# Optimization experiments

Measured on AMD Instinct MI355X. Metric: run time of the kernel, lower is better.

Reference implementation:

```python
import jax, jax.numpy as jnp
import numpy as np
from jax import lax

# LiteMSA config: in_ch=256, out_ch=256, dim=8, heads=32, total_dim=256, scales=(3,)
DIM = 8
QKV_CH = 768          # 3 * total_dim
PW_GROUPS = 96        # 3 * heads


def setup_inputs() -> dict:
    key = jax.random.key(0)
    ks = jax.random.split(key, 5)
    x = jax.random.normal(ks[0], (16, 256, 64, 64), jnp.float32)
    w_qkv = jax.random.normal(ks[1], (768, 256), jnp.float32) * 0.02      # 1x1 conv
    w_dw = jax.random.normal(ks[2], (768, 1, 3, 3), jnp.float32) * 0.02   # depthwise 3x3
    w_pw = jax.random.normal(ks[3], (768, 8, 1, 1), jnp.float32) * 0.02   # grouped 1x1, 96 groups
    w_proj = jax.random.normal(ks[4], (256, 512), jnp.float32) * 0.02     # 1x1 conv
    bn_gamma = jnp.ones((256,), jnp.float32)
    bn_beta = jnp.zeros((256,), jnp.float32)
    bn_mean = jnp.zeros((256,), jnp.float32)
    bn_var = jnp.ones((256,), jnp.float32)
    return {"x": x, "w_qkv": w_qkv, "w_dw": w_dw, "w_pw": w_pw, "w_proj": w_proj,
            "bn_gamma": bn_gamma, "bn_beta": bn_beta, "bn_mean": bn_mean, "bn_var": bn_var}


def reference(x, w_qkv, w_dw, w_pw, w_proj, bn_gamma, bn_beta, bn_mean, bn_var):
    B, _, H, W = x.shape
    dn = ("NCHW", "OIHW", "NCHW")
    # qkv 1x1 conv
    qkv = jnp.einsum("bchw,oc->bohw", x, w_qkv)  # [B,768,H,W]
    # multi-scale aggregation: depthwise 3x3 -> grouped 1x1
    agg = lax.conv_general_dilated(qkv, w_dw, (1, 1), "SAME",
                                   dimension_numbers=dn, feature_group_count=QKV_CH)
    agg = lax.conv_general_dilated(agg, w_pw, (1, 1), "SAME",
                                   dimension_numbers=dn, feature_group_count=PW_GROUPS)
    ms = jnp.concatenate([qkv, agg], axis=1)  # [B,1536,H,W]
    # [B, heads_total=64, N=H*W, 3*dim]
    ms = ms.reshape(B, -1, 3 * DIM, H * W).transpose(0, 1, 3, 2)
    q = jax.nn.relu(ms[..., :DIM])
    k = jax.nn.relu(ms[..., DIM:2 * DIM])
    v = ms[..., 2 * DIM:]
    # pad v with ones for normalizer channel
    v = jnp.concatenate([v, jnp.ones(v.shape[:-1] + (1,), v.dtype)], axis=-1)  # [B,h,N,dim+1]
    kv = jnp.einsum("bhnd,bhne->bhde", k, v)   # [B,h,dim,dim+1]
    out = jnp.einsum("bhnd,bhde->bhne", q, kv)  # [B,h,N,dim+1]
    out = out[..., :DIM] / (out[..., DIM:] + 1e-15)
    out = out.transpose(0, 1, 3, 2).reshape(B, -1, H, W)  # [B,512,H,W]
    # proj 1x1 conv + BatchNorm (inference, running stats)
    y = jnp.einsum("bchw,oc->bohw", out, w_proj)
    inv = bn_gamma / jnp.sqrt(bn_var + 1e-5)
    y = y * inv[None, :, None, None] + (bn_beta - bn_mean * inv)[None, :, None, None]
    return y
```

## Files before the change

### kernel.cpp

```cpp
#include <hip/hip_runtime.h>
#include <hip/hip_bf16.h>


#define NB 16
#define CQKV 768
#define P4096 4096
#define QFIX_CAP (1u << 21)

typedef __bf16 bf16x8 __attribute__((ext_vector_type(8)));
typedef float f32x4 __attribute__((ext_vector_type(4)));

#define MFMA_BF16 __builtin_amdgcn_mfma_f32_16x16x32_bf16

__device__ __forceinline__ ushort f2bf(float f) {
    union { float f; unsigned int u; } x; x.f = f;
    unsigned int u = x.u;
    unsigned int r = (u + 0x7FFFu + ((u >> 16) & 1u)) >> 16;
    return (ushort)r;
}
__device__ __forceinline__ float bf2f(ushort u) {
    union { unsigned int u; float f; } x; x.u = ((unsigned int)u) << 16;
    return x.f;
}
__device__ __forceinline__ unsigned int pk2bf(float x, float y) {
    __hip_bfloat162 h = __float22bfloat162_rn(make_float2(x, y));
    union { __hip_bfloat162 b; unsigned int u; } c; c.b = h; return c.u;
}
__device__ __forceinline__ void stage_hi8(const float* v, ushort* dh) {
    union { unsigned int u[4]; uint4 q; } H;
    #pragma unroll
    for (int i = 0; i < 4; i++) H.u[i] = pk2bf(v[2 * i], v[2 * i + 1]);
    *(uint4*)dh = H.q;
}

__device__ __forceinline__ void gload16(void* lds, const void* g) {
    __builtin_amdgcn_global_load_lds(
        (const __attribute__((address_space(1))) void*)g,
        (__attribute__((address_space(3))) void*)lds, 16, 0, 0);
}

__global__ __launch_bounds__(128) void conv_w(
    const float* __restrict__ W, ushort* __restrict__ Ah, ushort* __restrict__ Al)
{
    const int rv = blockIdx.x;
    const int t  = threadIdx.x;
    int phys;
    if (rv < 256) phys = (rv >> 3) * 24 + (rv & 7);
    else { int r2 = rv - 256; phys = (r2 >> 4) * 24 + 8 + (r2 & 15); }
    int c = t * 2;
    float w0 = W[(size_t)phys * 256 + c];
    float w1 = W[(size_t)phys * 256 + c + 1];
    unsigned int h = pk2bf(w0, w1);
    float f0 = __uint_as_float(h << 16);
    float f1 = __uint_as_float(h & 0xffff0000u);
    unsigned int l = pk2bf(w0 - f0, w1 - f1);
    int sl = ((c >> 3) & 3) ^ ((rv >> 1) & 3);
    int idx = (c & ~31) + sl * 8 + (c & 7);
    *(unsigned int*)&Ah[(size_t)rv * 256 + idx] = h;
    *(unsigned int*)&Al[(size_t)rv * 256 + idx] = l;
}

__global__ __launch_bounds__(256) void conv_x(
    const float* __restrict__ X, ushort* __restrict__ XTh, ushort* __restrict__ XTl)
{
    const int pt = blockIdx.x;
    const int ct = blockIdx.y;
    const int b  = blockIdx.z;
    const int t  = threadIdx.x;
    const int p0 = pt * 64, c0 = ct * 64;

    __shared__ float tile[64][65];

    {
        int cr = t >> 2, pc = (t & 3) * 16;
        const float* xr = X + ((size_t)b * 256 + c0 + cr) * P4096 + p0 + pc;
        float4 v0 = *(const float4*)xr;
        float4 v1 = *(const float4*)(xr + 4);
        float4 v2 = *(const float4*)(xr + 8);
        float4 v3 = *(const float4*)(xr + 12);
        float* d = &tile[cr][pc];
        d[0]=v0.x; d[1]=v0.y; d[2]=v0.z; d[3]=v0.w;
        d[4]=v1.x; d[5]=v1.y; d[6]=v1.z; d[7]=v1.w;
        d[8]=v2.x; d[9]=v2.y; d[10]=v2.z; d[11]=v2.w;
        d[12]=v3.x; d[13]=v3.y; d[14]=v3.z; d[15]=v3.w;
    }
    __syncthreads();

    #pragma unroll
    for (int pass = 0; pass < 2; pass++) {
        int tp = t >> 2;
        int cc = (t & 3) + pass * 4;
        int p  = p0 + tp;
        float v[8];
        #pragma unroll
        for (int j = 0; j < 8; j++) v[j] = tile[cc * 8 + j][tp];
        union { unsigned int u[4]; uint4 q; } H, L;
        #pragma unroll
        for (int i = 0; i < 4; i++) {
            unsigned int h = pk2bf(v[2 * i], v[2 * i + 1]);
            H.u[i] = h;
            float f0 = __uint_as_float(h << 16);
            float f1 = __uint_as_float(h & 0xffff0000u);
            L.u[i] = pk2bf(v[2 * i] - f0, v[2 * i + 1] - f1);
        }
        int c = c0 + cc * 8;
        int sl = ((c >> 3) & 3) ^ ((p >> 1) & 3);
        size_t idx = ((size_t)b * P4096 + p) * 256 + (c & ~31) + sl * 8;
        *(uint4*)&XTh[idx] = H.q;
        *(uint4*)&XTl[idx] = L.q;
    }
}

__global__ void zero_cnt(unsigned int* qmeta) { if (threadIdx.x == 0) qmeta[0] = 0; }

__global__ __launch_bounds__(256, 2) void gemm_fused(
    const ushort* __restrict__ Ah, const ushort* __restrict__ Al,
    const ushort* __restrict__ Bh, const ushort* __restrict__ Bl,
    ushort* __restrict__ Cbf, float* __restrict__ qplane,
    unsigned int* __restrict__ qmeta)
{
    const int hw = blockIdx.x;
    const int lg = (hw & 7) * 384 + (hw >> 3);
    const int mt = lg % 6;
    const int rem = lg / 6;
    const int n0 = (rem & 31) * 128;
    const int b  = rem >> 5;
    const int t  = threadIdx.x;
    const int wave = t >> 6, lane = t & 63, quad = lane >> 4, l15 = lane & 15;
    const int wr = wave >> 1, wc = wave & 1;
    const int M0 = mt * 128;

    __shared__ __align__(16) ushort AsH[2][4096];
    __shared__ __align__(16) ushort AsL[2][4096];
    __shared__ __align__(16) ushort BsH[2][4096];
    __shared__ __align__(16) ushort BsL[2][4096];

    int aoff[4], boff[4];
    #pragma unroll
    for (int i = 0; i < 4; i++) {
        int ra = wr * 64 + i * 16 + l15;
        aoff[i] = ra * 64 + ((quad ^ ((ra >> 1) & 3)) << 4);
        int rb = wc * 64 + i * 16 + l15;
        boff[i] = rb * 64 + ((quad ^ ((rb >> 1) & 3)) << 4);
    }

    const int srow = t >> 2;
    const int schunk = (t & 3) * 8;
    const size_t abase = (size_t)(M0 + srow) * 256 + schunk;
    const size_t bbase = ((size_t)b * P4096 + n0 + srow) * 256 + schunk;
    const int ldsoff = wave * 1024;

    f32x4 acc[4][4];
    #pragma unroll
    for (int mi = 0; mi < 4; mi++)
        #pragma unroll
        for (int nj = 0; nj < 4; nj++)
            #pragma unroll
            for (int r = 0; r < 4; r++) acc[mi][nj][r] = 0.0f;

    if (mt < 2) {
        auto stageQ = [&](int d, int kw) {
            #pragma unroll
            for (int i = 0; i < 2; i++) {
                int lo = ldsoff + i * 4096;
                size_t so = (size_t)(i * 64) * 256 + (size_t)kw * 32;
                gload16((char*)AsH[d] + lo, Ah + abase + so);
                gload16((char*)AsL[d] + lo, Al + abase + so);
                gload16((char*)BsH[d] + lo, Bh + bbase + so);
                gload16((char*)BsL[d] + lo, Bl + bbase + so);
            }
        };
        stageQ(0, 0);
        for (int kw = 0; kw < 8; kw++) {
            int cur = kw & 1;
            if (kw < 7) {
                stageQ(cur ^ 1, kw + 1);
                asm volatile("s_waitcnt vmcnt(8)" ::: "memory");
            } else {
                asm volatile("s_waitcnt vmcnt(0)" ::: "memory");
            }
            __builtin_amdgcn_s_barrier();
            bf16x8 ah[4], al[4];
            #pragma unroll
            for (int mi = 0; mi < 4; mi++) {
                ah[mi] = *(const bf16x8*)((const char*)AsH[cur] + aoff[mi]);
                al[mi] = *(const bf16x8*)((const char*)AsL[cur] + aoff[mi]);
            }
            #pragma unroll
            for (int nj = 0; nj < 4; nj++) {
                bf16x8 bh = *(const bf16x8*)((const char*)BsH[cur] + boff[nj]);
                bf16x8 bl = *(const bf16x8*)((const char*)BsL[cur] + boff[nj]);
                #pragma unroll
                for (int mi = 0; mi < 4; mi++) {
                    acc[mi][nj] = MFMA_BF16(ah[mi], bh, acc[mi][nj], 0, 0, 0);
                    acc[mi][nj] = MFMA_BF16(al[mi], bh, acc[mi][nj], 0, 0, 0);
                    acc[mi][nj] = MFMA_BF16(ah[mi], bl, acc[mi][nj], 0, 0, 0);
                }
            }
            __builtin_amdgcn_s_barrier();
        }
        unsigned int* qlist = qmeta + 16;
        #pragma unroll
        for (int mi = 0; mi < 4; mi++)
            #pragma unroll
            for (int nj = 0; nj < 4; nj++)
                #pragma unroll
                for (int r = 0; r < 4; r++) {
                    int rv = M0 + wr * 64 + mi * 16 + quad * 4 + r;
                    int rp = (rv >> 3) * 24 + (rv & 7);
                    int col = n0 + wc * 64 + nj * 16 + l15;
                    float v = acc[mi][nj][r];
                    Cbf[((size_t)b * CQKV + rp) * P4096 + col] = f2bf(v);
                    qplane[((size_t)b * 256 + rv) * P4096 + col] = v;
                    if (fabsf(v) < 1e-4f) {
                        unsigned int idx = atomicAdd(qmeta, 1u);
                        if (idx < QFIX_CAP)
                            qlist[idx] = (unsigned int)(((b * 256 + rv) << 12) | col);
                    }
                }
    } else {
        auto stageKV = [&](int d, int kw) {
            #pragma unroll
            for (int i = 0; i < 2; i++) {
                int lo = ldsoff + i * 4096;
                size_t so = (size_t)(i * 64) * 256 + (size_t)kw * 32;
                gload16((char*)AsH[d] + lo, Ah + abase + so);
                gload16((char*)BsH[d] + lo, Bh + bbase + so);
            }
        };
        stageKV(0, 0);
        for (int kw = 0; kw < 8; kw++) {
            int cur = kw & 1;
            if (kw < 7) {
                stageKV(cur ^ 1, kw + 1);
                asm volatile("s_waitcnt vmcnt(4)" ::: "memory");
            } else {
                asm volatile("s_waitcnt vmcnt(0)" ::: "memory");
            }
            __builtin_amdgcn_s_barrier();
            bf16x8 ah[4];
            #pragma unroll
            for (int mi = 0; mi < 4; mi++)
                ah[mi] = *(const bf16x8*)((const char*)AsH[cur] + aoff[mi]);
            #pragma unroll
            for (int nj = 0; nj < 4; nj++) {
                bf16x8 bh = *(const bf16x8*)((const char*)BsH[cur] + boff[nj]);
                #pragma unroll
                for (int mi = 0; mi < 4; mi++)
                    acc[mi][nj] = MFMA_BF16(ah[mi], bh, acc[mi][nj], 0, 0, 0);
            }
            __builtin_amdgcn_s_barrier();
        }
        #pragma unroll
        for (int mi = 0; mi < 4; mi++)
            #pragma unroll
            for (int nj = 0; nj < 4; nj++)
                #pragma unroll
                for (int r = 0; r < 4; r++) {
                    int rv2 = (M0 - 256) + wr * 64 + mi * 16 + quad * 4 + r;
                    int rp = (rv2 >> 4) * 24 + 8 + (rv2 & 15);
                    int col = n0 + wc * 64 + nj * 16 + l15;
                    Cbf[((size_t)b * CQKV + rp) * P4096 + col] = f2bf(acc[mi][nj][r]);
                }
    }
}

__global__ __launch_bounds__(256) void qfix2_kernel(
    float* __restrict__ qplane, const float* __restrict__ w_qkv,
    const float* __restrict__ x, const unsigned int* __restrict__ qmeta)
{
    unsigned int n = qmeta[0];
    if (n > QFIX_CAP) n = QFIX_CAP;
    const unsigned int* list = qmeta + 16;
    const int wave = threadIdx.x >> 6, lane = threadIdx.x & 63;
    for (unsigned int e = blockIdx.x * 4 + wave; e < n; e += gridDim.x * 4) {
        unsigned int i = list[e];
        int p   = (int)(i & 4095);
        int qch = (int)((i >> 12) & 255);
        int b   = (int)(i >> 20);
        int row = (qch >> 3) * 24 + (qch & 7);
        const float* wr = w_qkv + (size_t)row * 256;
        const float* xr = x + (size_t)b * 256 * P4096 + p;
        double s = 0.0;
        #pragma unroll
        for (int j = 0; j < 4; j++) {
            int c = lane * 4 + j;
            s += (double)wr[c] * (double)xr[(size_t)c * P4096];
        }
        #pragma unroll
        for (int off = 32; off > 0; off >>= 1) s += __shfl_xor(s, off, 64);
        if (lane == 0)
            qplane[((size_t)(b * 256 + qch)) * P4096 + p] = (float)s;
    }
}

__global__ __launch_bounds__(512, 8) void dwpw_kernel(
    const ushort* __restrict__ qkv, const float* __restrict__ wdw,
    const float* __restrict__ wpw, ushort* __restrict__ agg)
{
    const int rt = blockIdx.x;
    const int g  = blockIdx.y;
    const int b  = blockIdx.z;
    const int t  = threadIdx.x;
    const int r0 = rt * 16;
    const int cg = g * 8;

    __shared__ __align__(16) ushort tile[8][18][80];

    const ushort* src = qkv + ((size_t)(b * CQKV + cg)) * P4096;

    if (t < 288) {
        int ch = t / 36;
        int rr = (t % 36) >> 1;
        int side = t & 1;
        *(uint4*)&tile[ch][rr][side * 72] = make_uint4(0, 0, 0, 0);
    }
    #pragma unroll
    for (int i = 0; i < 3; i++) {
        int id = t + i * 512;
        if (id < 1152) {
            int ch  = id / 144;
            int rem = id - ch * 144;
            int rr  = rem >> 3;
            int oct = (rem & 7) * 8;
            int grow = r0 - 1 + rr;
            uint4 v = make_uint4(0, 0, 0, 0);
            if (grow >= 0 && grow < 64)
                v = *(const uint4*)(src + (size_t)ch * P4096 + (size_t)grow * 64 + oct);
            *(uint4*)&tile[ch][rr][8 + oct] = v;
        }
    }
    __syncthreads();

    const int kc  = t & 31;
    const int row = t >> 5;
    const float* wdwg = wdw + (size_t)cg * 9;
    const float* wpwg = wpw + (size_t)cg * 8;

    float acc0[8], acc1[8];
    #pragma unroll
    for (int oi = 0; oi < 8; oi++) { acc0[oi] = 0.0f; acc1[oi] = 0.0f; }

    #pragma unroll
    for (int c = 0; c < 8; c++) {
        float dv0 = 0.0f, dv1 = 0.0f;
        #pragma unroll
        for (int dy = 0; dy < 3; dy++) {
            const ushort* rp = &tile[c][row + dy][2 * kc + 4];
            unsigned int u1 = *(const unsigned int*)(rp + 2);
            unsigned int u2 = *(const unsigned int*)(rp + 4);
            unsigned int u3 = *(const unsigned int*)(rp + 6);
            float xm1 = __uint_as_float(u1 & 0xffff0000u);
            float x0  = __uint_as_float(u2 << 16);
            float x1  = __uint_as_float(u2 & 0xffff0000u);
            float x2  = __uint_as_float(u3 << 16);
            float w0 = wdwg[c * 9 + dy * 3 + 0];
            float w1 = wdwg[c * 9 + dy * 3 + 1];
            float w2 = wdwg[c * 9 + dy * 3 + 2];
            dv0 = fmaf(w0, xm1, dv0); dv0 = fmaf(w1, x0, dv0); dv0 = fmaf(w2, x1, dv0);
            dv1 = fmaf(w0, x0,  dv1); dv1 = fmaf(w1, x1, dv1); dv1 = fmaf(w2, x2, dv1);
        }
        #pragma unroll
        for (int oi = 0; oi < 8; oi++) {
            float w = wpwg[oi * 8 + c];
            acc0[oi] = fmaf(w, dv0, acc0[oi]);
            acc1[oi] = fmaf(w, dv1, acc1[oi]);
        }
    }

    size_t obase = ((size_t)(b * CQKV + cg)) * P4096 + (size_t)(r0 + row) * 64 + 2 * kc;
    #pragma unroll
    for (int oi = 0; oi < 8; oi++) {
        unsigned int u = (unsigned int)f2bf(acc0[oi]) |
                         ((unsigned int)f2bf(acc1[oi]) << 16);
        *(unsigned int*)&agg[obase + (size_t)oi * P4096] = u;
    }
}

__global__ __launch_bounds__(256) void kv_kernel(
    const ushort* __restrict__ qkv, const ushort* __restrict__ agg,
    float* __restrict__ kv)
{
    const int h = blockIdx.x, b = blockIdx.y, t = threadIdx.x;
    const ushort* src = (h < 32)
        ? qkv + ((size_t)(b * CQKV + h * 24)) * P4096
        : agg + ((size_t)(b * CQKV + (h - 32) * 24)) * P4096;

    float acc[72];
    #pragma unroll
    for (int i = 0; i < 72; i++) acc[i] = 0.0f;

    for (int pi = 0; pi < 16; pi++) {
        int p = t + pi * 256;
        float kvv[8], vv[8];
        #pragma unroll
        for (int d = 0; d < 8; d++) {
            float xk = bf2f(src[(size_t)(8 + d) * P4096 + p]);
            kvv[d] = xk > 0.0f ? xk : 0.0f;
        }
        #pragma unroll
        for (int e = 0; e < 8; e++) vv[e] = bf2f(src[(size_t)(16 + e) * P4096 + p]);
        #pragma unroll
        for (int d = 0; d < 8; d++) {
            #pragma unroll
            for (int e = 0; e < 8; e++) acc[d * 9 + e] += kvv[d] * vv[e];
            acc[d * 9 + 8] += kvv[d];
        }
    }

    #pragma unroll
    for (int i = 0; i < 72; i++) {
        float v = acc[i];
        #pragma unroll
        for (int off = 32; off > 0; off >>= 1) v += __shfl_xor(v, off, 64);
        acc[i] = v;
    }
    __shared__ float part[4][72];
    int wave = t >> 6, lane = t & 63;
    if (lane == 0) {
        #pragma unroll
        for (int i = 0; i < 72; i++) part[wave][i] = acc[i];
    }
    __syncthreads();
    if (t < 72)
        kv[((size_t)b * 64 + h) * 72 + t] = part[0][t] + part[1][t] + part[2][t] + part[3][t];
}

__global__ __launch_bounds__(256) void attn_out_kernel(
    const float* __restrict__ qplane, ushort* __restrict__ agg,
    const float* __restrict__ kv)
{
    const int pt = blockIdx.x, h = blockIdx.y, b = blockIdx.z, t = threadIdx.x;
    __shared__ float kvs[72];
    if (t < 72) kvs[t] = kv[((size_t)b * 64 + h) * 72 + t];
    __syncthreads();

    const bool lohead = (h < 32);
    const float* srcf = lohead
        ? qplane + ((size_t)(b * 256 + h * 8)) * P4096 : nullptr;
    const ushort* srcb = lohead ? nullptr
        : agg + ((size_t)(b * CQKV + (h - 32) * 24)) * P4096;

    int p = pt * 256 + t;
    float num[8]; float den = 0.0f;
    #pragma unroll
    for (int e = 0; e < 8; e++) num[e] = 0.0f;
    #pragma unroll
    for (int d = 0; d < 8; d++) {
        float q = lohead ? srcf[(size_t)d * P4096 + p]
                         : bf2f(srcb[(size_t)d * P4096 + p]);
        q = q > 0.0f ? q : 0.0f;
        #pragma unroll
        for (int e = 0; e < 8; e++) num[e] += q * kvs[d * 9 + e];
        den += q * kvs[d * 9 + 8];
    }
    float rd = 1.0f / (den + 1e-15f);
    ushort* dst = agg + ((size_t)(b * CQKV + (h / 2) * 24 + 8 + (h % 2) * 8)) * P4096 + p;
    #pragma unroll
    for (int e = 0; e < 8; e++)
        dst[(size_t)e * P4096] = f2bf(num[e] * rd);
}

__global__ __launch_bounds__(256) void gemm_proj(
    const float* __restrict__ A,
    const ushort* __restrict__ Bagg,
    float* __restrict__ Y,
    const float* __restrict__ bn_g, const float* __restrict__ bn_b,
    const float* __restrict__ bn_m, const float* __restrict__ bn_v)
{
    const int n0 = blockIdx.x * 64;
    const int m0 = blockIdx.y * 64;
    const int b  = blockIdx.z;
    const int t  = threadIdx.x;
    const int wave = t >> 6, lane = t & 63, quad = lane >> 4, l15 = lane & 15;

    __shared__ __align__(16) ushort As[64][40];
    __shared__ __align__(16) ushort Bs[64][40];

    f32x4 acc[4];
    #pragma unroll
    for (int nt = 0; nt < 4; nt++)
        #pragma unroll
        for (int r = 0; r < 4; r++) acc[nt][r] = 0.0f;

    const int am = t >> 2, ak = (t & 3) * 8;
    const int bn = t & 63, kg = (t >> 6) * 8;

    for (int k0 = 0; k0 < 512; k0 += 32) {
        float av[8];
        *(float4*)&av[0] = *(const float4*)(A + (size_t)(m0 + am) * 512 + k0 + ak);
        *(float4*)&av[4] = *(const float4*)(A + (size_t)(m0 + am) * 512 + k0 + ak + 4);
        ushort bu[8];
        #pragma unroll
        for (int i = 0; i < 8; i++) {
            int kk = k0 + kg + i;
            int amch = (kk >> 4) * 24 + 8 + (kk & 15);
            bu[i] = Bagg[((size_t)b * CQKV + amch) * P4096 + n0 + bn];
        }

        __syncthreads();
        stage_hi8(av, &As[am][ak]);
        {
            union { ushort us[8]; uint4 q; } Bp;
            #pragma unroll
            for (int i = 0; i < 8; i++) Bp.us[i] = bu[i];
            *(uint4*)&Bs[bn][kg] = Bp.q;
        }
        __syncthreads();

        bf16x8 af = *(const bf16x8*)&As[wave * 16 + l15][quad * 8];
        #pragma unroll
        for (int nt = 0; nt < 4; nt++) {
            bf16x8 bf = *(const bf16x8*)&Bs[nt * 16 + l15][quad * 8];
            acc[nt] = MFMA_BF16(af, bf, acc[nt], 0, 0, 0);
        }
    }

    #pragma unroll
    for (int nt = 0; nt < 4; nt++) {
        #pragma unroll
        for (int r = 0; r < 4; r++) {
            int row = m0 + wave * 16 + quad * 4 + r;
            int col = n0 + nt * 16 + l15;
            float inv = bn_g[row] / sqrtf(bn_v[row] + 1e-5f);
            float v = acc[nt][r] * inv + (bn_b[row] - bn_m[row] * inv);
            Y[((size_t)b * 256 + row) * P4096 + col] = v;
        }
    }
}

extern "C" void kernel_launch(void* const* d_in, const int* in_sizes, int n_in,
                              void* d_out, int out_size, void* d_ws, size_t ws_size,
                              hipStream_t stream) {
    const float* x      = (const float*)d_in[0];
    const float* w_qkv  = (const float*)d_in[1];
    const float* w_dw   = (const float*)d_in[2];
    const float* w_pw   = (const float*)d_in[3];
    const float* w_proj = (const float*)d_in[4];
    const float* bn_g   = (const float*)d_in[5];
    const float* bn_b   = (const float*)d_in[6];
    const float* bn_m   = (const float*)d_in[7];
    const float* bn_v   = (const float*)d_in[8];
    float* y = (float*)d_out;

    char* ws = (char*)d_ws;
    ushort* qkv_bf = (ushort*)(ws);
    float*  qplane = (float*) (ws + 100663296);
    ushort* agg_bf = (ushort*)(ws + 167772160);
    ushort* XTh = (ushort*)(ws + 167772160);
    ushort* XTl = (ushort*)(ws + 167772160 + 33554432);
    ushort* Awh = (ushort*)(ws + 167772160 + 67108864);
    ushort* Awl = (ushort*)(ws + 167772160 + 67108864 + 393216);
    float*  kvbuf  = (float*)d_out;
    unsigned int* qmeta = (unsigned int*)((char*)d_out + 524288);

    conv_w<<<dim3(768), 128, 0, stream>>>(w_qkv, Awh, Awl);
    zero_cnt<<<1, 64, 0, stream>>>(qmeta);
    conv_x<<<dim3(64, 4, NB), 256, 0, stream>>>(x, XTh, XTl);

    gemm_fused<<<dim3(3072), 256, 0, stream>>>(
        Awh, Awl, XTh, XTl, qkv_bf, qplane, qmeta);

    qfix2_kernel<<<dim3(1024), 256, 0, stream>>>(qplane, w_qkv, x, qmeta);

    dwpw_kernel<<<dim3(4, 96, NB), 512, 0, stream>>>(qkv_bf, w_dw, w_pw, agg_bf);

    kv_kernel<<<dim3(64, NB), 256, 0, stream>>>(qkv_bf, agg_bf, kvbuf);

    attn_out_kernel<<<dim3(16, 64, NB), 256, 0, stream>>>(qplane, agg_bf, kvbuf);

    gemm_proj<<<dim3(64, 4, NB), 256, 0, stream>>>(
        w_proj, agg_bf, y, bn_g, bn_b, bn_m, bn_v);
}
```

Baseline: 411.3 us.

## Retile projection GEMM to 128x128 with double-buffered LDS and pre-converted weights

```diff
diff --git a/kernel.cpp b/kernel.cpp
--- a/kernel.cpp
+++ b/kernel.cpp
@@ -25,12 +25,6 @@
 __device__ __forceinline__ unsigned int pk2bf(float x, float y) {
     __hip_bfloat162 h = __float22bfloat162_rn(make_float2(x, y));
     union { __hip_bfloat162 b; unsigned int u; } c; c.b = h; return c.u;
-}
-__device__ __forceinline__ void stage_hi8(const float* v, ushort* dh) {
-    union { unsigned int u[4]; uint4 q; } H;
-    #pragma unroll
-    for (int i = 0; i < 4; i++) H.u[i] = pk2bf(v[2 * i], v[2 * i + 1]);
-    *(uint4*)dh = H.q;
 }
 
 __device__ __forceinline__ void gload16(void* lds, const void* g) {
@@ -58,6 +52,20 @@
     int idx = (c & ~31) + sl * 8 + (c & 7);
     *(unsigned int*)&Ah[(size_t)rv * 256 + idx] = h;
     *(unsigned int*)&Al[(size_t)rv * 256 + idx] = l;
+}
+
+__global__ __launch_bounds__(256) void conv_wp(
+    const float* __restrict__ W, ushort* __restrict__ Awp)
+{
+    const int m = blockIdx.x;
+    const int t = threadIdx.x;
+    int c = t * 2;
+    float w0 = W[(size_t)m * 512 + c];
+    float w1 = W[(size_t)m * 512 + c + 1];
+    unsigned int h = pk2bf(w0, w1);
+    int sl = ((c >> 3) & 3) ^ ((m >> 1) & 3);
+    int idx = (c & ~31) + sl * 8 + (c & 7);
+    *(unsigned int*)&Awp[(size_t)m * 512 + idx] = h;
 }
 
 __global__ __launch_bounds__(256) void conv_x(
@@ -461,72 +469,118 @@
         dst[(size_t)e * P4096] = f2bf(num[e] * rd);
 }
 
-__global__ __launch_bounds__(256) void gemm_proj(
-    const float* __restrict__ A,
+__global__ __launch_bounds__(256, 2) void gemm_proj(
+    const ushort* __restrict__ Awp,
     const ushort* __restrict__ Bagg,
     float* __restrict__ Y,
     const float* __restrict__ bn_g, const float* __restrict__ bn_b,
     const float* __restrict__ bn_m, const float* __restrict__ bn_v)
 {
-    const int n0 = blockIdx.x * 64;
-    const int m0 = blockIdx.y * 64;
-    const int b  = blockIdx.z;
+    const int hw = blockIdx.x;
+    const int lg = (hw & 7) * 128 + (hw >> 3);
+    const int mt = lg & 1;
+    const int rem = lg >> 1;
+    const int n0 = (rem & 31) * 128;
+    const int b  = rem >> 5;
     const int t  = threadIdx.x;
     const int wave = t >> 6, lane = t & 63, quad = lane >> 4, l15 = lane & 15;
-
-    __shared__ __align__(16) ushort As[64][40];
-    __shared__ __align__(16) ushort Bs[64][40];
-
-    f32x4 acc[4];
-    #pragma unroll
-    for (int nt = 0; nt < 4; nt++)
-        #pragma unroll
-        for (int r = 0; r < 4; r++) acc[nt][r] = 0.0f;
-
-    const int am = t >> 2, ak = (t & 3) * 8;
-    const int bn = t & 63, kg = (t >> 6) * 8;
-
-    for (int k0 = 0; k0 < 512; k0 += 32) {
-        float av[8];
-        *(float4*)&av[0] = *(const float4*)(A + (size_t)(m0 + am) * 512 + k0 + ak);
-        *(float4*)&av[4] = *(const float4*)(A + (size_t)(m0 + am) * 512 + k0 + ak + 4);
-        ushort bu[8];
-        #pragma unroll
-        for (int i = 0; i < 8; i++) {
-            int kk = k0 + kg + i;
-            int amch = (kk >> 4) * 24 + 8 + (kk & 15);
-            bu[i] = Bagg[((size_t)b * CQKV + amch) * P4096 + n0 + bn];
-        }
-
-        __syncthreads();
-        stage_hi8(av, &As[am][ak]);
-        {
-            union { ushort us[8]; uint4 q; } Bp;
-            #pragma unroll
-            for (int i = 0; i < 8; i++) Bp.us[i] = bu[i];
-            *(uint4*)&Bs[bn][kg] = Bp.q;
-        }
-        __syncthreads();
-
-        bf16x8 af = *(const bf16x8*)&As[wave * 16 + l15][quad * 8];
-        #pragma unroll
-        for (int nt = 0; nt < 4; nt++) {
-            bf16x8 bf = *(const bf16x8*)&Bs[nt * 16 + l15][quad * 8];
-            acc[nt] = MFMA_BF16(af, bf, acc[nt], 0, 0, 0);
-        }
-    }
-
-    #pragma unroll
-    for (int nt = 0; nt < 4; nt++) {
-        #pragma unroll
-        for (int r = 0; r < 4; r++) {
-            int row = m0 + wave * 16 + quad * 4 + r;
-            int col = n0 + nt * 16 + l15;
-            float inv = bn_g[row] / sqrtf(bn_v[row] + 1e-5f);
-            float v = acc[nt][r] * inv + (bn_b[row] - bn_m[row] * inv);
-            Y[((size_t)b * 256 + row) * P4096 + col] = v;
-        }
-    }
+    const int wr = wave >> 1, wc = wave & 1;
+    const int M0 = mt * 128;
+
+    __shared__ __align__(16) ushort As[2][4096];
+    __shared__ __align__(16) ushort Bs[2][5120];
+
+    int aoff[4], boff[4];
+    #pragma unroll
+    for (int i = 0; i < 4; i++) {
+        int ra = wr * 64 + i * 16 + l15;
+        aoff[i] = ra * 64 + ((quad ^ ((ra >> 1) & 3)) << 4);
+        int rb = wc * 64 + i * 16 + l15;
+        boff[i] = rb * 80 + quad * 16;
+    }
+
+    const int arow0 = t >> 2, achk = (t & 3) * 8;
+    const size_t abase = (size_t)(M0 + arow0) * 512 + achk;
+    const size_t abase1 = (size_t)(M0 + 64 + arow0) * 512 + achk;
+    const int ldsoffA = wave * 1024;
+
+    const int bn_ = t & 127, half = t >> 7;
+    const size_t bchanstride = (size_t)P4096;
+
+    f32x4 acc[4][4];
+    #pragma unroll
+    for (int mi = 0; mi < 4; mi++)
+        #pragma unroll
+        for (int nj = 0; nj < 4; nj++)
+            #pragma unroll
+            for (int r = 0; r < 4; r++) acc[mi][nj][r] = 0.0f;
+
+    auto stageA = [&](int d, int kw) {
+        gload16((char*)As[d] + ldsoffA,        Awp + abase  + (size_t)kw * 32);
+        gload16((char*)As[d] + ldsoffA + 4096, Awp + abase1 + (size_t)kw * 32);
+    };
+    ushort bu[16];
+    auto loadB = [&](int kw) {
+        const ushort* bsrc = Bagg
+            + ((size_t)b * CQKV + (size_t)(kw * 2 + half) * 24 + 8) * P4096
+            + n0 + bn_;
+        #pragma unroll
+        for (int j = 0; j < 16; j++) bu[j] = bsrc[(size_t)j * bchanstride];
+    };
+    auto writeB = [&](int d) {
+        union { ushort us[8]; uint4 q; } P0, P1;
+        #pragma unroll
+        for (int j = 0; j < 8; j++) { P0.us[j] = bu[j]; P1.us[j] = bu[8 + j]; }
+        ushort* dst = &Bs[d][bn_ * 40 + half * 16];
+        *(uint4*)dst = P0.q;
+        *(uint4*)(dst + 8) = P1.q;
+    };
+
+    stageA(0, 0);
+    loadB(0);
+    asm volatile("s_waitcnt vmcnt(0)" ::: "memory");
+    writeB(0);
+    asm volatile("s_waitcnt lgkmcnt(0)" ::: "memory");
+    __builtin_amdgcn_s_barrier();
+
+    for (int kw = 0; kw < 16; kw++) {
+        int cur = kw & 1;
+        if (kw < 15) {
+            stageA(cur ^ 1, kw + 1);
+            loadB(kw + 1);
+        }
+        bf16x8 af[4];
+        #pragma unroll
+        for (int mi = 0; mi < 4; mi++)
+            af[mi] = *(const bf16x8*)((const char*)As[cur] + aoff[mi]);
+        #pragma unroll
+        for (int nj = 0; nj < 4; nj++) {
+            bf16x8 bf = *(const bf16x8*)((const char*)Bs[cur] + boff[nj]);
+            #pragma unroll
+            for (int mi = 0; mi < 4; mi++)
+                acc[mi][nj] = MFMA_BF16(af[mi], bf, acc[mi][nj], 0, 0, 0);
+        }
+        __builtin_amdgcn_s_barrier();
+        if (kw < 15) {
+            asm volatile("s_waitcnt vmcnt(0)" ::: "memory");
+            writeB(cur ^ 1);
+            asm volatile("s_waitcnt lgkmcnt(0)" ::: "memory");
+        }
+        __builtin_amdgcn_s_barrier();
+    }
+
+    #pragma unroll
+    for (int mi = 0; mi < 4; mi++)
+        #pragma unroll
+        for (int nj = 0; nj < 4; nj++)
+            #pragma unroll
+            for (int r = 0; r < 4; r++) {
+                int row = M0 + wr * 64 + mi * 16 + quad * 4 + r;
+                int col = n0 + wc * 64 + nj * 16 + l15;
+                float inv = bn_g[row] / sqrtf(bn_v[row] + 1e-5f);
+                float v = acc[mi][nj][r] * inv + (bn_b[row] - bn_m[row] * inv);
+                Y[((size_t)b * 256 + row) * P4096 + col] = v;
+            }
 }
 
 extern "C" void kernel_launch(void* const* d_in, const int* in_sizes, int n_in,
@@ -551,6 +605,7 @@
     ushort* XTl = (ushort*)(ws + 167772160 + 33554432);
     ushort* Awh = (ushort*)(ws + 167772160 + 67108864);
     ushort* Awl = (ushort*)(ws + 167772160 + 67108864 + 393216);
+    ushort* Awp = (ushort*)(ws + 100663296);
     float*  kvbuf  = (float*)d_out;
     unsigned int* qmeta = (unsigned int*)((char*)d_out + 524288);
 
@@ -569,6 +624,8 @@
 
     attn_out_kernel<<<dim3(16, 64, NB), 256, 0, stream>>>(qplane, agg_bf, kvbuf);
 
-    gemm_proj<<<dim3(64, 4, NB), 256, 0, stream>>>(
-        w_proj, agg_bf, y, bn_g, bn_b, bn_m, bn_v);
-}
+    conv_wp<<<dim3(256), 256, 0, stream>>>(w_proj, Awp);
+
+    gemm_proj<<<dim3(1024), 256, 0, stream>>>(
+        Awp, agg_bf, y, bn_g, bn_b, bn_m, bn_v);
+}
```

After: 396.6 us. 3.6% less time.
